# Kernel optimization log

Hardware: AMD Instinct MI355X
Metric: run time of the kernel (lower is better)

## Reference

```python
import jax, jax.numpy as jnp
import numpy as np

B = 2          # graphs (images)
GRID = 13      # patches per spatial dim -> N = 169 patches per image
N = GRID * GRID
NN = B * N     # total nodes
C = 256        # hidden_dim / out_channels per head
H = 4          # attention heads
L = 3          # GAT layers
LRELU_SLOPE = 0.2
LN_EPS = 1e-5


def _dense_edges():
    # fully-connected directed graph (i != j) per image, as in create_graph
    idx = np.arange(N)
    src, dst = np.meshgrid(idx, idx, indexing='ij')
    mask = src != dst
    src, dst = src[mask], dst[mask]              # [N*(N-1)]
    offs = (np.arange(B) * N)[:, None]
    e_src = (src[None, :] + offs).reshape(-1)
    e_dst = (dst[None, :] + offs).reshape(-1)
    return e_src.astype(np.int32), e_dst.astype(np.int32)


def setup_inputs() -> dict:
    key = jax.random.key(0)
    ks = jax.random.split(key, 8)
    s = 0.05
    e_src, e_dst = _dense_edges()
    return {
        'x':   jax.random.normal(ks[0], (NN, C), jnp.float32),
        'Wl':  jax.random.normal(ks[1], (L, C, H * C), jnp.float32) * s,
        'bl':  jnp.zeros((L, H * C), jnp.float32),
        'Wr':  jax.random.normal(ks[2], (L, C, H * C), jnp.float32) * s,
        'br':  jnp.zeros((L, H * C), jnp.float32),
        'att': jax.random.normal(ks[3], (L, H, C), jnp.float32) * s,
        'bias': jnp.zeros((L, C), jnp.float32),
        'ln_g': jnp.ones((L, C), jnp.float32),
        'ln_b': jnp.zeros((L, C), jnp.float32),
        'W1':  jax.random.normal(ks[4], (L, C, 2 * C), jnp.float32) * s,
        'b1':  jnp.zeros((L, 2 * C), jnp.float32),
        'W2':  jax.random.normal(ks[5], (L, 2 * C, C), jnp.float32) * s,
        'b2':  jnp.zeros((L, C), jnp.float32),
        'edge_src': jnp.asarray(e_src),
        'edge_dst': jnp.asarray(e_dst),
        'batch_ids': jnp.repeat(jnp.arange(B, dtype=jnp.int32), N),
    }


def _gatv2(x, Wl, bl, Wr, br, att, bias, src, dst, n_nodes):
    # PyG GATv2Conv, concat=False (mean over heads)
    xl = (x @ Wl + bl).reshape(n_nodes, H, C)   # source transform
    xr = (x @ Wr + br).reshape(n_nodes, H, C)   # target transform
    e = jax.nn.leaky_relu(xl[src] + xr[dst], LRELU_SLOPE)     # [E,H,C]
    logits = jnp.einsum('ehc,hc->eh', e, att)                 # [E,H]
    m = jax.ops.segment_max(logits, dst, num_segments=n_nodes)
    a = jnp.exp(logits - m[dst])
    z = jax.ops.segment_sum(a, dst, num_segments=n_nodes)
    alpha = a / (z[dst] + 1e-16)                              # softmax per target
    msg = alpha[:, :, None] * xl[src]                         # [E,H,C]
    agg = jax.ops.segment_sum(msg, dst, num_segments=n_nodes) # [N,H,C]
    return agg.mean(axis=1) + bias


def _layernorm(x, g, b):
    mu = x.mean(-1, keepdims=True)
    var = jnp.mean((x - mu) ** 2, -1, keepdims=True)
    return (x - mu) * jax.lax.rsqrt(var + LN_EPS) * g + b


def reference(x, Wl, bl, Wr, br, att, bias, ln_g, ln_b, W1, b1, W2, b2,
              edge_src, edge_dst, batch_ids):
    n_nodes = x.shape[0]
    for l in range(L):
        residual = x
        h = _gatv2(x, Wl[l], bl[l], Wr[l], br[l], att[l], bias[l],
                   edge_src, edge_dst, n_nodes)
        h = _layernorm(h, ln_g[l], ln_b[l])
        mlp = jnp.maximum(h @ W1[l] + b1[l], 0.0) @ W2[l] + b2[l]
        x = residual + mlp
    # global mean pool per graph
    sums = jax.ops.segment_sum(x, batch_ids, num_segments=B)
    cnts = jax.ops.segment_sum(jnp.ones((n_nodes, 1), x.dtype), batch_ids,
                               num_segments=B)
    return sums / cnts
```

## Files before the change

### kernel.cpp

```cpp
#include <hip/hip_runtime.h>
#include <hip/hip_bf16.h>

typedef __hip_bfloat16 bf16;
typedef __attribute__((ext_vector_type(8))) short short8v;
typedef __attribute__((ext_vector_type(4))) float float4v;

#define NNODES 169
#define NNTOT  338
#define CH     256
#define NH     4
#define NL     3
#define SPAD   176
#define LN_EPS 1e-5f

__device__ __forceinline__ float b2f(bf16 v) { return __bfloat162float(v); }
__device__ __forceinline__ float lrelu(float v) { return fmaxf(v, 0.2f * v); }
__device__ __forceinline__ float ldm(const void* p, size_t i, int isbf) {
    return isbf ? b2f(((const bf16*)p)[i]) : ((const float*)p)[i];
}
__device__ __forceinline__ short f2bf(float f) {
    union { float f; unsigned u; } x; x.f = f;
    return (short)((x.u + 0x7FFFu + ((x.u >> 16) & 1u)) >> 16);
}
__device__ __forceinline__ int sniff_bf(const void* lng) {
    return ((((const unsigned*)lng)[0] & 0xFFFFu) == 0x3F80u) ? 1 : 0;
}

__global__ __launch_bounds__(256) void k_wt(
    const void* __restrict__ Wl, const void* __restrict__ Wr,
    const void* __restrict__ W1, const void* __restrict__ W2,
    short* __restrict__ wlT, short* __restrict__ wrT,
    short* __restrict__ w1T, short* __restrict__ w2T,
    const void* __restrict__ lng)
{
    __shared__ float s_t[32][33];
    const int isbf = sniff_bf(lng);
    const int z = blockIdx.z, mat = z & 3, l = z >> 2;
    const void* src; short* dst; int K, N;
    if      (mat == 0) { src = Wl; dst = wlT; K = CH;     N = NH * CH; }
    else if (mat == 1) { src = Wr; dst = wrT; K = CH;     N = NH * CH; }
    else if (mat == 2) { src = W1; dst = w1T; K = CH;     N = 2 * CH;  }
    else               { src = W2; dst = w2T; K = 2 * CH; N = CH;      }
    const int tiles = (K >> 5) * (N >> 5);
    if ((int)blockIdx.x >= tiles) return;
    const int tn = blockIdx.x % (N >> 5), tk = blockIdx.x / (N >> 5);
    const int k0 = tk * 32, n0 = tn * 32;
    const size_t lKN = (size_t)l * K * N;
    const int tx = threadIdx.x & 31, ty = threadIdx.x >> 5;

    for (int r = ty; r < 32; r += 8)
        s_t[r][tx] = ldm(src, lKN + (size_t)(k0 + r) * N + n0 + tx, isbf);
    __syncthreads();
    for (int r = ty; r < 32; r += 8)
        dst[lKN + (size_t)(n0 + r) * K + k0 + tx] = f2bf(s_t[tx][r]);
}

template<int ACT, int RES, int XLT>
__device__ __forceinline__ void mfma_gemm(
    const void* __restrict__ Av, int a_bf,
    const short* __restrict__ WT,
    const void* __restrict__ bv_, size_t oB, int isbf,
    const void* __restrict__ x_res, int r_bf,
    float* __restrict__ out, float* __restrict__ xlT,
    int M, int K, int N, int row0, int col0)
{
    __shared__ short sA[64 * 40];
    __shared__ short sBT[64 * 40];
    const int tid = threadIdx.x, lane = tid & 63, w = tid >> 6;
    const int arow = tid >> 2, akoff = (tid & 3) * 8;
    const int m = lane & 15, kb = (lane >> 4) * 8;
    const int w16 = w * 16;

    float4v acc[4];
    #pragma unroll
    for (int t = 0; t < 4; t++) acc[t] = (float4v){0.f, 0.f, 0.f, 0.f};

    for (int k0 = 0; k0 < K; k0 += 32) {
        short av8[8];
        const int gr = row0 + arow;
        if (gr < M) {
            const size_t ai = (size_t)gr * K + k0 + akoff;
            if (a_bf) {
                *(int4*)av8 = *(const int4*)((const bf16*)Av + ai);
            } else {
                const float4 f0 = *(const float4*)((const float*)Av + ai);
                const float4 f1 = *(const float4*)((const float*)Av + ai + 4);
                av8[0] = f2bf(f0.x); av8[1] = f2bf(f0.y);
                av8[2] = f2bf(f0.z); av8[3] = f2bf(f0.w);
                av8[4] = f2bf(f1.x); av8[5] = f2bf(f1.y);
                av8[6] = f2bf(f1.z); av8[7] = f2bf(f1.w);
            }
        } else {
            #pragma unroll
            for (int j = 0; j < 8; j++) av8[j] = 0;
        }
        short bv8[8];
        *(int4*)bv8 = *(const int4*)(WT + (size_t)(col0 + arow) * K + k0 + akoff);
        __syncthreads();
        *(short8v*)&sA[arow * 40 + akoff]  = *(short8v*)av8;
        *(short8v*)&sBT[arow * 40 + akoff] = *(short8v*)bv8;
        __syncthreads();
        const short8v af = *(const short8v*)&sA[(w16 + m) * 40 + kb];
        #pragma unroll
        for (int t = 0; t < 4; t++) {
            const short8v bf = *(const short8v*)&sBT[(t * 16 + m) * 40 + kb];
            acc[t] = __builtin_amdgcn_mfma_f32_16x16x32_bf16(af, bf, acc[t], 0, 0, 0);
        }
    }

    const int rq = (lane >> 4) * 4;
    #pragma unroll
    for (int t = 0; t < 4; t++) {
        const int col = col0 + t * 16 + m;
        const float bias_v = ldm(bv_, oB + col, isbf);
        #pragma unroll
        for (int r = 0; r < 4; r++) {
            const int gr = row0 + w16 + rq + r;
            if (gr >= M) continue;
            float v = acc[t][r] + bias_v;
            if (ACT) v = fmaxf(v, 0.f);
            if (RES) v += ldm(x_res, (size_t)gr * N + col, r_bf);
            out[(size_t)gr * N + col] = v;
            if (XLT) {
                const int hh = col >> 8, cc = col & 255;
                const int gg = (gr >= NNODES) ? 1 : 0;
                const int ss = gr - gg * NNODES;
                xlT[((size_t)(gg * NH + hh) * CH + cc) * SPAD + ss] = v;
            }
        }
    }
}

__global__ __launch_bounds__(256) void k_gemm_lr(
    const void* __restrict__ Av, int israw,
    const short* __restrict__ wlT, const short* __restrict__ wrT, size_t oWT,
    const void* __restrict__ bl, const void* __restrict__ br, size_t oB,
    float* __restrict__ xl, float* __restrict__ xr, float* __restrict__ xlT,
    const void* __restrict__ lng)
{
    const int isbf = sniff_bf(lng);
    const int a_bf = israw ? isbf : 0;
    const int row0 = blockIdx.x * 64, col0 = blockIdx.y * 64;
    if (blockIdx.z == 0)
        mfma_gemm<0,0,1>(Av, a_bf, wlT + oWT, bl, oB, isbf, nullptr, 0,
                         xl, xlT, NNTOT, CH, NH * CH, row0, col0);
    else
        mfma_gemm<0,0,0>(Av, a_bf, wrT + oWT, br, oB, isbf, nullptr, 0,
                         xr, nullptr, NNTOT, CH, NH * CH, row0, col0);
}

__global__ __launch_bounds__(256) void k_mlp1(
    const float* __restrict__ A, const short* __restrict__ w1T, size_t oWT,
    const void* __restrict__ b, size_t oB,
    float* __restrict__ out, const void* __restrict__ lng)
{
    const int isbf = sniff_bf(lng);
    mfma_gemm<1,0,0>(A, 0, w1T + oWT, b, oB, isbf, nullptr, 0,
                     out, nullptr, NNTOT, CH, 2 * CH, blockIdx.x * 64, blockIdx.y * 64);
}

__global__ __launch_bounds__(256) void k_mlp2(
    const float* __restrict__ A, const short* __restrict__ w2T, size_t oWT,
    const void* __restrict__ b, size_t oB,
    const void* __restrict__ x_res, int israw,
    float* __restrict__ out, const void* __restrict__ lng)
{
    const int isbf = sniff_bf(lng);
    const int r_bf = israw ? isbf : 0;
    mfma_gemm<0,1,0>(A, 0, w2T + oWT, b, oB, isbf, x_res, r_bf,
                     out, nullptr, NNTOT, 2 * CH, CH, blockIdx.x * 64, blockIdx.y * 64);
}

__global__ __launch_bounds__(256) void k_logits_sm(
    const float* __restrict__ xlT, const float* __restrict__ xr,
    const void* __restrict__ att, size_t oA,
    float* __restrict__ alphaR, const void* __restrict__ lng)
{
    __shared__ float s_att[CH];
    __shared__ float s_xr[4 * CH];
    __shared__ float s_tile[32 * SPAD];
    __shared__ float s_log[4 * SPAD];
    const int isbf = sniff_bf(lng);
    const int g = blockIdx.z, h = blockIdx.y, d0 = blockIdx.x * 4;
    const int tid = threadIdx.x, lane = tid & 63, wv = tid >> 6;

    s_att[tid] = ldm(att, oA + h * CH + tid, isbf);
    #pragma unroll
    for (int i = 0; i < 4; i++) {
        const int d = d0 + i;
        s_xr[i * CH + tid] = (d < NNODES)
            ? xr[(size_t)(g * NNODES + d) * (NH * CH) + h * CH + tid] : 0.f;
    }

    float l0 = 0.f, l1 = 0.f, l2 = 0.f, l3 = 0.f;
    const int s = tid;
    const float4* src = (const float4*)(xlT + ((size_t)(g * NH + h) * CH) * SPAD);
    for (int ch = 0; ch < 8; ch++) {
        __syncthreads();
        for (int i = tid; i < 32 * SPAD / 4; i += 256)
            ((float4*)s_tile)[i] = src[ch * (32 * SPAD / 4) + i];
        __syncthreads();
        if (s < NNODES) {
            const int cb = ch * 32;
            #pragma unroll
            for (int c = 0; c < 32; c++) {
                const float v = s_tile[c * SPAD + s];
                const float a = s_att[cb + c];
                l0 += a * lrelu(v + s_xr[cb + c]);
                l1 += a * lrelu(v + s_xr[CH + cb + c]);
                l2 += a * lrelu(v + s_xr[2 * CH + cb + c]);
                l3 += a * lrelu(v + s_xr[3 * CH + cb + c]);
            }
        }
    }
    if (s < NNODES) {
        s_log[s] = l0; s_log[SPAD + s] = l1;
        s_log[2 * SPAD + s] = l2; s_log[3 * SPAD + s] = l3;
    }
    __syncthreads();

    {
        const int d = d0 + wv;
        const float* row = s_log + wv * SPAD;
        const int s0 = lane, s1 = lane + 64, s2 = lane + 128;
        const float v0 = (s0 < NNODES && s0 != d) ? row[s0] : -1e30f;
        const float v1 = (s1 < NNODES && s1 != d) ? row[s1] : -1e30f;
        const float v2 = (s2 < NNODES && s2 != d) ? row[s2] : -1e30f;
        float mx = fmaxf(v0, fmaxf(v1, v2));
        mx = fmaxf(mx, __shfl_xor(mx, 32)); mx = fmaxf(mx, __shfl_xor(mx, 16));
        mx = fmaxf(mx, __shfl_xor(mx, 8));  mx = fmaxf(mx, __shfl_xor(mx, 4));
        mx = fmaxf(mx, __shfl_xor(mx, 2));  mx = fmaxf(mx, __shfl_xor(mx, 1));
        const float e0 = expf(v0 - mx), e1 = expf(v1 - mx), e2 = expf(v2 - mx);
        float z = e0 + e1 + e2;
        z += __shfl_xor(z, 32); z += __shfl_xor(z, 16); z += __shfl_xor(z, 8);
        z += __shfl_xor(z, 4);  z += __shfl_xor(z, 2);  z += __shfl_xor(z, 1);
        const float sc = 0.25f / (z + 1e-16f);
        if (d < NNODES) {
            float* arow = alphaR + ((size_t)(g * NH + h) * NNODES + d) * SPAD;
            if (s0 < NNODES) arow[s0] = e0 * sc;
            if (s1 < NNODES) arow[s1] = e1 * sc;
            if (s2 < NNODES) arow[s2] = e2 * sc;
        }
    }
}

__global__ __launch_bounds__(256) void k_agg(
    const float* __restrict__ alphaR, const float* __restrict__ xl,
    float* __restrict__ part)
{
    __shared__ float s_a[32 * 33];
    __shared__ float s_x[32 * 64];
    const int gh = blockIdx.z, g = gh >> 2, h = gh & 3;
    const int d0 = blockIdx.x * 32, c0 = blockIdx.y * 64;
    const int tid = threadIdx.x;
    const int dr = (tid >> 4) * 2, cq = (tid & 15) * 4;
    const int sr = tid >> 3, sc4 = (tid & 7) * 4;
    const int xc8 = (tid & 7) * 8;

    float acc[2][4] = {{0.f,0.f,0.f,0.f},{0.f,0.f,0.f,0.f}};

    for (int s0 = 0; s0 < NNODES; s0 += 32) {
        __syncthreads();
        {
            const int d = d0 + sr;
            const float* ap = alphaR + ((size_t)gh * NNODES + d) * SPAD + s0 + sc4;
            const int ok = (d < NNODES);
            s_a[sr * 33 + sc4 + 0] = (ok && s0 + sc4 + 0 < NNODES) ? ap[0] : 0.f;
            s_a[sr * 33 + sc4 + 1] = (ok && s0 + sc4 + 1 < NNODES) ? ap[1] : 0.f;
            s_a[sr * 33 + sc4 + 2] = (ok && s0 + sc4 + 2 < NNODES) ? ap[2] : 0.f;
            s_a[sr * 33 + sc4 + 3] = (ok && s0 + sc4 + 3 < NNODES) ? ap[3] : 0.f;
        }
        {
            const int sg = s0 + sr;
            if (sg < NNODES) {
                const float* xp = xl + (size_t)(g * NNODES + sg) * (NH * CH) + h * CH + c0 + xc8;
                *(float4*)&s_x[sr * 64 + xc8]     = *(const float4*)(xp);
                *(float4*)&s_x[sr * 64 + xc8 + 4] = *(const float4*)(xp + 4);
            } else {
                #pragma unroll
                for (int j = 0; j < 8; j++) s_x[sr * 64 + xc8 + j] = 0.f;
            }
        }
        __syncthreads();
        #pragma unroll
        for (int k = 0; k < 32; k++) {
            const float a0 = s_a[(dr + 0) * 33 + k];
            const float a1 = s_a[(dr + 1) * 33 + k];
            const float4 xv = *(const float4*)&s_x[k * 64 + cq];
            acc[0][0] += a0 * xv.x; acc[0][1] += a0 * xv.y;
            acc[0][2] += a0 * xv.z; acc[0][3] += a0 * xv.w;
            acc[1][0] += a1 * xv.x; acc[1][1] += a1 * xv.y;
            acc[1][2] += a1 * xv.z; acc[1][3] += a1 * xv.w;
        }
    }
    #pragma unroll
    for (int i = 0; i < 2; i++) {
        const int d = d0 + dr + i;
        if (d >= NNODES) continue;
        float4 v;
        v.x = acc[i][0]; v.y = acc[i][1]; v.z = acc[i][2]; v.w = acc[i][3];
        *(float4*)(part + ((size_t)h * NNTOT + g * NNODES + d) * CH + c0 + cq) = v;
    }
}

__global__ __launch_bounds__(256) void k_ln(
    const float* __restrict__ part,
    const void* __restrict__ bias, size_t oB,
    const void* __restrict__ ln_g, size_t oG,
    const void* __restrict__ ln_b, size_t oBt,
    float* __restrict__ h_out, const void* __restrict__ lng)
{
    __shared__ float s_red[8];
    const int isbf = sniff_bf(lng);
    const int node = blockIdx.x, c = threadIdx.x;
    const int lane = c & 63, wv = c >> 6;

    float vch = part[((size_t)0 * NNTOT + node) * CH + c]
              + part[((size_t)1 * NNTOT + node) * CH + c]
              + part[((size_t)2 * NNTOT + node) * CH + c]
              + part[((size_t)3 * NNTOT + node) * CH + c]
              + ldm(bias, oB + c, isbf);

    float s1 = vch, s2 = vch * vch;
    s1 += __shfl_xor(s1, 32); s2 += __shfl_xor(s2, 32);
    s1 += __shfl_xor(s1, 16); s2 += __shfl_xor(s2, 16);
    s1 += __shfl_xor(s1, 8);  s2 += __shfl_xor(s2, 8);
    s1 += __shfl_xor(s1, 4);  s2 += __shfl_xor(s2, 4);
    s1 += __shfl_xor(s1, 2);  s2 += __shfl_xor(s2, 2);
    s1 += __shfl_xor(s1, 1);  s2 += __shfl_xor(s2, 1);
    if (lane == 0) { s_red[wv] = s1; s_red[4 + wv] = s2; }
    __syncthreads();
    const float S1 = s_red[0] + s_red[1] + s_red[2] + s_red[3];
    const float S2 = s_red[4] + s_red[5] + s_red[6] + s_red[7];
    const float mu  = S1 * (1.f / CH);
    const float var = S2 * (1.f / CH) - mu * mu;
    const float o = (vch - mu) * rsqrtf(var + LN_EPS) * ldm(ln_g, oG + c, isbf)
                  + ldm(ln_b, oBt + c, isbf);
    h_out[(size_t)node * CH + c] = o;
}

__global__ __launch_bounds__(256) void k_pool(const float* __restrict__ x,
                                              void* __restrict__ out,
                                              const void* __restrict__ lng) {
    const int isbf = sniff_bf(lng);
    const int g = blockIdx.x, c = threadIdx.x;
    float s = 0.f;
    const float* p = x + (size_t)g * NNODES * CH + c;
    for (int n = 0; n < NNODES; n++) s += p[(size_t)n * CH];
    const float v = s * (1.f / NNODES);
    if (isbf) ((bf16*)out)[g * CH + c] = __float2bfloat16(v);
    else      ((float*)out)[g * CH + c] = v;
}

extern "C" void kernel_launch(void* const* d_in, const int* in_sizes, int n_in,
                              void* d_out, int out_size, void* d_ws, size_t ws_size,
                              hipStream_t stream)
{
    const void* x_in = d_in[0];
    const void* Wl   = d_in[1];
    const void* bl   = d_in[2];
    const void* Wr   = d_in[3];
    const void* br   = d_in[4];
    const void* att  = d_in[5];
    const void* bias = d_in[6];
    const void* lng  = d_in[7];
    const void* lnb  = d_in[8];
    const void* W1   = d_in[9];
    const void* b1   = d_in[10];
    const void* W2   = d_in[11];
    const void* b2   = d_in[12];

    float* ws     = (float*)d_ws;
    float* xl     = ws;
    float* xr     = xl + (size_t)NNTOT * NH * CH;
    float* xlT    = xr + (size_t)NNTOT * NH * CH;
    float* alphaR = xlT + (size_t)2 * NH * CH * SPAD;
    float* part   = alphaR + (size_t)2 * NH * NNODES * SPAD;
    float* h_ln   = part + (size_t)NH * NNTOT * CH;
    float* m1     = h_ln + (size_t)NNTOT * CH;
    float* xa     = m1 + (size_t)NNTOT * 2 * CH;
    float* xb     = xa + (size_t)NNTOT * CH;
    short* wlT    = (short*)(xb + (size_t)NNTOT * CH);
    short* wrT    = wlT + (size_t)NL * CH * NH * CH;
    short* w1T    = wrT + (size_t)NL * CH * NH * CH;
    short* w2T    = w1T + (size_t)NL * CH * 2 * CH;

    const size_t sB  = NH * CH;
    const size_t sA  = NH * CH;
    const size_t sC  = CH;
    const size_t sB1 = 2 * CH;
    const size_t sWT  = (size_t)CH * NH * CH;
    const size_t sW1T = (size_t)CH * 2 * CH;
    const size_t sW2T = (size_t)2 * CH * CH;

    k_wt<<<dim3(256, 1, 12), 256, 0, stream>>>(
        Wl, Wr, W1, W2, wlT, wrT, w1T, w2T, lng);

    const void* x_l[3] = { x_in, xa, xb };
    float*      x_o[3] = { xa, xb, xa };

    for (int l = 0; l < NL; l++) {
        const int israw = (l == 0);
        k_gemm_lr<<<dim3(6, 16, 2), 256, 0, stream>>>(
            x_l[l], israw, wlT, wrT, (size_t)l * sWT,
            bl, br, (size_t)l * sB, xl, xr, xlT, lng);
        k_logits_sm<<<dim3(43, NH, 2), 256, 0, stream>>>(
            xlT, xr, att, (size_t)l * sA, alphaR, lng);
        k_agg<<<dim3(6, 4, 8), 256, 0, stream>>>(alphaR, xl, part);
        k_ln<<<dim3(NNTOT), 256, 0, stream>>>(
            part, bias, (size_t)l * sC, lng, (size_t)l * sC, lnb, (size_t)l * sC,
            h_ln, lng);
        k_mlp1<<<dim3(6, 8), 256, 0, stream>>>(
            h_ln, w1T, (size_t)l * sW1T, b1, (size_t)l * sB1, m1, lng);
        k_mlp2<<<dim3(6, 4), 256, 0, stream>>>(
            m1, w2T, (size_t)l * sW2T, b2, (size_t)l * sC,
            x_l[l], israw, x_o[l], lng);
    }

    k_pool<<<dim3(2), 256, 0, stream>>>(xa, d_out, lng);
}
```

Measured before the change: 345.7 us.

## Stage full-K GEMM tiles in LDS once and enlarge logits tile chunks

The MFMA GEMM helper now loads the entire K extent of its A and B tiles into shared memory in a single pass. The per-32 K-step loop with two barriers per iteration is replaced by one barrier and a fully unrolled MFMA loop, with K made a template parameter. The logits kernel moves its xlT staging to 64-channel chunks, halving the number of load and sync rounds, and the pool loop gains an unroll pragma. The cost is much larger LDS use per block (about 66 KB for the mlp2 kernel), which can reduce occupancy and removes overlap between global loads and MFMA work.

```diff
diff --git a/kernel.cpp b/kernel.cpp
--- a/kernel.cpp
+++ b/kernel.cpp
@@ -55,56 +55,70 @@
         dst[lKN + (size_t)(n0 + r) * K + k0 + tx] = f2bf(s_t[tx][r]);
 }
 
-template<int ACT, int RES, int XLT>
+template<int KK, int ACT, int RES, int XLT>
 __device__ __forceinline__ void mfma_gemm(
+    short* __restrict__ sA, short* __restrict__ sBT,
     const void* __restrict__ Av, int a_bf,
     const short* __restrict__ WT,
     const void* __restrict__ bv_, size_t oB, int isbf,
     const void* __restrict__ x_res, int r_bf,
     float* __restrict__ out, float* __restrict__ xlT,
-    int M, int K, int N, int row0, int col0)
-{
-    __shared__ short sA[64 * 40];
-    __shared__ short sBT[64 * 40];
+    int M, int N, int row0, int col0)
+{
+    const int STR = KK + 8;
     const int tid = threadIdx.x, lane = tid & 63, w = tid >> 6;
-    const int arow = tid >> 2, akoff = (tid & 3) * 8;
+    const int r = tid >> 2, q = tid & 3;
+    const int kseg = KK / 4, kb0 = q * kseg;
     const int m = lane & 15, kb = (lane >> 4) * 8;
     const int w16 = w * 16;
+
+    {
+        const int gr = row0 + r;
+        const int ok = (gr < M);
+        if (a_bf) {
+            const bf16* ap = (const bf16*)Av + (size_t)gr * KK + kb0;
+            #pragma unroll
+            for (int j = 0; j < kseg; j += 8) {
+                int4 v = ok ? *(const int4*)(ap + j) : make_int4(0, 0, 0, 0);
+                *(int4*)&sA[r * STR + kb0 + j] = v;
+            }
+        } else {
+            const float* ap = (const float*)Av + (size_t)gr * KK + kb0;
+            #pragma unroll
+            for (int j = 0; j < kseg; j += 8) {
+                short v8[8];
+                if (ok) {
+                    const float4 f0 = *(const float4*)(ap + j);
+                    const float4 f1 = *(const float4*)(ap + j + 4);
+                    v8[0] = f2bf(f0.x); v8[1] = f2bf(f0.y);
+                    v8[2] = f2bf(f0.z); v8[3] = f2bf(f0.w);
+                    v8[4] = f2bf(f1.x); v8[5] = f2bf(f1.y);
+                    v8[6] = f2bf(f1.z); v8[7] = f2bf(f1.w);
+                } else {
+                    #pragma unroll
+                    for (int u = 0; u < 8; u++) v8[u] = 0;
+                }
+                *(int4*)&sA[r * STR + kb0 + j] = *(int4*)v8;
+            }
+        }
+        const short* bp = WT + (size_t)(col0 + r) * KK + kb0;
+        #pragma unroll
+        for (int j = 0; j < kseg; j += 8)
+            *(int4*)&sBT[r * STR + kb0 + j] = *(const int4*)(bp + j);
+    }
+    __syncthreads();
 
     float4v acc[4];
     #pragma unroll
     for (int t = 0; t < 4; t++) acc[t] = (float4v){0.f, 0.f, 0.f, 0.f};
 
-    for (int k0 = 0; k0 < K; k0 += 32) {
-        short av8[8];
-        const int gr = row0 + arow;
-        if (gr < M) {
-            const size_t ai = (size_t)gr * K + k0 + akoff;
-            if (a_bf) {
-                *(int4*)av8 = *(const int4*)((const bf16*)Av + ai);
-            } else {
-                const float4 f0 = *(const float4*)((const float*)Av + ai);
-                const float4 f1 = *(const float4*)((const float*)Av + ai + 4);
-                av8[0] = f2bf(f0.x); av8[1] = f2bf(f0.y);
-                av8[2] = f2bf(f0.z); av8[3] = f2bf(f0.w);
-                av8[4] = f2bf(f1.x); av8[5] = f2bf(f1.y);
-                av8[6] = f2bf(f1.z); av8[7] = f2bf(f1.w);
-            }
-        } else {
-            #pragma unroll
-            for (int j = 0; j < 8; j++) av8[j] = 0;
-        }
-        short bv8[8];
-        *(int4*)bv8 = *(const int4*)(WT + (size_t)(col0 + arow) * K + k0 + akoff);
-        __syncthreads();
-        *(short8v*)&sA[arow * 40 + akoff]  = *(short8v*)av8;
-        *(short8v*)&sBT[arow * 40 + akoff] = *(short8v*)bv8;
-        __syncthreads();
-        const short8v af = *(const short8v*)&sA[(w16 + m) * 40 + kb];
+    #pragma unroll
+    for (int kc = 0; kc < KK / 32; kc++) {
+        const short8v af = *(const short8v*)&sA[(w16 + m) * STR + kc * 32 + kb];
         #pragma unroll
         for (int t = 0; t < 4; t++) {
-            const short8v bf = *(const short8v*)&sBT[(t * 16 + m) * 40 + kb];
-            acc[t] = __builtin_amdgcn_mfma_f32_16x16x32_bf16(af, bf, acc[t], 0, 0, 0);
+            const short8v bfv = *(const short8v*)&sBT[(t * 16 + m) * STR + kc * 32 + kb];
+            acc[t] = __builtin_amdgcn_mfma_f32_16x16x32_bf16(af, bfv, acc[t], 0, 0, 0);
         }
     }
 
@@ -114,10 +128,10 @@
         const int col = col0 + t * 16 + m;
         const float bias_v = ldm(bv_, oB + col, isbf);
         #pragma unroll
-        for (int r = 0; r < 4; r++) {
-            const int gr = row0 + w16 + rq + r;
+        for (int rr = 0; rr < 4; rr++) {
+            const int gr = row0 + w16 + rq + rr;
             if (gr >= M) continue;
-            float v = acc[t][r] + bias_v;
+            float v = acc[t][rr] + bias_v;
             if (ACT) v = fmaxf(v, 0.f);
             if (RES) v += ldm(x_res, (size_t)gr * N + col, r_bf);
             out[(size_t)gr * N + col] = v;
@@ -138,15 +152,17 @@
     float* __restrict__ xl, float* __restrict__ xr, float* __restrict__ xlT,
     const void* __restrict__ lng)
 {
+    __shared__ short sA[64 * 264];
+    __shared__ short sBT[64 * 264];
     const int isbf = sniff_bf(lng);
     const int a_bf = israw ? isbf : 0;
     const int row0 = blockIdx.x * 64, col0 = blockIdx.y * 64;
     if (blockIdx.z == 0)
-        mfma_gemm<0,0,1>(Av, a_bf, wlT + oWT, bl, oB, isbf, nullptr, 0,
-                         xl, xlT, NNTOT, CH, NH * CH, row0, col0);
+        mfma_gemm<256,0,0,1>(sA, sBT, Av, a_bf, wlT + oWT, bl, oB, isbf,
+                             nullptr, 0, xl, xlT, NNTOT, NH * CH, row0, col0);
     else
-        mfma_gemm<0,0,0>(Av, a_bf, wrT + oWT, br, oB, isbf, nullptr, 0,
-                         xr, nullptr, NNTOT, CH, NH * CH, row0, col0);
+        mfma_gemm<256,0,0,0>(sA, sBT, Av, a_bf, wrT + oWT, br, oB, isbf,
+                             nullptr, 0, xr, nullptr, NNTOT, NH * CH, row0, col0);
 }
 
 __global__ __launch_bounds__(256) void k_mlp1(
@@ -154,9 +170,11 @@
     const void* __restrict__ b, size_t oB,
     float* __restrict__ out, const void* __restrict__ lng)
 {
-    const int isbf = sniff_bf(lng);
-    mfma_gemm<1,0,0>(A, 0, w1T + oWT, b, oB, isbf, nullptr, 0,
-                     out, nullptr, NNTOT, CH, 2 * CH, blockIdx.x * 64, blockIdx.y * 64);
+    __shared__ short sA[64 * 264];
+    __shared__ short sBT[64 * 264];
+    const int isbf = sniff_bf(lng);
+    mfma_gemm<256,1,0,0>(sA, sBT, A, 0, w1T + oWT, b, oB, isbf, nullptr, 0,
+                         out, nullptr, NNTOT, 2 * CH, blockIdx.x * 64, blockIdx.y * 64);
 }
 
 __global__ __launch_bounds__(256) void k_mlp2(
@@ -165,10 +183,12 @@
     const void* __restrict__ x_res, int israw,
     float* __restrict__ out, const void* __restrict__ lng)
 {
+    __shared__ short sA[64 * 520];
+    __shared__ short sBT[64 * 520];
     const int isbf = sniff_bf(lng);
     const int r_bf = israw ? isbf : 0;
-    mfma_gemm<0,1,0>(A, 0, w2T + oWT, b, oB, isbf, x_res, r_bf,
-                     out, nullptr, NNTOT, 2 * CH, CH, blockIdx.x * 64, blockIdx.y * 64);
+    mfma_gemm<512,0,1,0>(sA, sBT, A, 0, w2T + oWT, b, oB, isbf, x_res, r_bf,
+                         out, nullptr, NNTOT, CH, blockIdx.x * 64, blockIdx.y * 64);
 }
 
 __global__ __launch_bounds__(256) void k_logits_sm(
@@ -178,7 +198,7 @@
 {
     __shared__ float s_att[CH];
     __shared__ float s_xr[4 * CH];
-    __shared__ float s_tile[32 * SPAD];
+    __shared__ float s_tile[64 * SPAD];
     __shared__ float s_log[4 * SPAD];
     const int isbf = sniff_bf(lng);
     const int g = blockIdx.z, h = blockIdx.y, d0 = blockIdx.x * 4;
@@ -195,15 +215,15 @@
     float l0 = 0.f, l1 = 0.f, l2 = 0.f, l3 = 0.f;
     const int s = tid;
     const float4* src = (const float4*)(xlT + ((size_t)(g * NH + h) * CH) * SPAD);
-    for (int ch = 0; ch < 8; ch++) {
+    for (int ch = 0; ch < 4; ch++) {
         __syncthreads();
-        for (int i = tid; i < 32 * SPAD / 4; i += 256)
-            ((float4*)s_tile)[i] = src[ch * (32 * SPAD / 4) + i];
+        for (int i = tid; i < 64 * SPAD / 4; i += 256)
+            ((float4*)s_tile)[i] = src[ch * (64 * SPAD / 4) + i];
         __syncthreads();
         if (s < NNODES) {
-            const int cb = ch * 32;
-            #pragma unroll
-            for (int c = 0; c < 32; c++) {
+            const int cb = ch * 64;
+            #pragma unroll 8
+            for (int c = 0; c < 64; c++) {
                 const float v = s_tile[c * SPAD + s];
                 const float a = s_att[cb + c];
                 l0 += a * lrelu(v + s_xr[cb + c]);
@@ -346,6 +366,7 @@
     const int g = blockIdx.x, c = threadIdx.x;
     float s = 0.f;
     const float* p = x + (size_t)g * NNODES * CH + c;
+    #pragma unroll 8
     for (int n = 0; n < NNODES; n++) s += p[(size_t)n * CH];
     const float v = s * (1.f / NNODES);
     if (isbf) ((bf16*)out)[g * CH + c] = __float2bfloat16(v);
```

New measurement: 321.8 us. 6.9% less time.
